# Kernel tuning notes

Hardware: AMD Instinct MI355X
Metric: run time of the kernel (lower is better)

Reference implementation:

```python
import jax, jax.numpy as jnp
import numpy as np

B = 1024
P = 8
D = 2048
NUM_IDS = 64
MARGIN = 0.3
EPS = 1e-12


def setup_inputs() -> dict:
    key = jax.random.key(0)
    k1, k2, k3 = jax.random.split(key, 3)
    feats = jax.random.normal(k1, (B, P * D), dtype=jnp.float32)
    labels = jax.random.randint(k2, (B,), 0, NUM_IDS, dtype=jnp.int64)
    subs = jax.random.randint(k3, (B,), 0, 2, dtype=jnp.int64)
    return {"feats": feats, "labels": labels, "subs": subs}


def reference(feats, labels, subs):
    b = feats.shape[0]
    f = feats.reshape(b, -1, D)  # [B, P, D]
    dt = f.dtype

    # Per-sample class centers via a single segment-mean pass
    # (equivalent to the original per-sample boolean-mask mean loop).
    seg_sum = jax.ops.segment_sum(f, labels, num_segments=NUM_IDS)  # [NUM_IDS, P, D]
    counts = jax.ops.segment_sum(jnp.ones((b,), dt), labels, num_segments=NUM_IDS)
    centers_by_id = seg_sum / jnp.maximum(counts, 1.0)[:, None, None]
    centers = centers_by_id[labels]  # [B, P, D]

    # dist_ap[i] = sum_p ||f[i,p] - center[i,p]||
    d_ap = jnp.sqrt(jnp.clip(jnp.sum((f - centers) ** 2, axis=-1), EPS, None)).sum(-1)  # [B]
    dist_ap = d_ap[:, None] + d_ap[None, :]  # [B, B]

    # pairwise_distance: dist_aa[i,j] = sum_p ||f[i,p] - f[j,p]||, via gemm trick
    sq = jnp.sum(f * f, axis=-1)  # [B, P]
    inner = jnp.einsum('ipd,jpd->ijp', f, f)  # [B, B, P]
    d2 = sq[:, None, :] + sq[None, :, :] - 2.0 * inner
    dist_aa = jnp.sqrt(jnp.clip(d2, EPS, None)).sum(-1)  # [B, B]

    # masked margin loss over negative (different-label) pairs
    mask = labels[:, None] != labels[None, :]  # [B, B] bool
    vals = jnp.clip(dist_ap - dist_aa + MARGIN, 0.0, None)
    maskf = mask.astype(dt)
    loss = jnp.sum(vals * maskf) / jnp.sum(maskf)
    return loss
```

## Files before the change

kernel.cpp:

```cpp
#include <hip/hip_runtime.h>
#include <hip/hip_bf16.h>

#define B_ 1024
#define P_ 8
#define D_ 2048
#define FD_ (P_ * D_)
#define NID 64
#define MARGIN_ 0.3f
#define EPS_ 1e-12f

typedef unsigned short u16;
typedef float float4_t __attribute__((ext_vector_type(4)));

#define AS1 __attribute__((address_space(1)))
#define AS3 __attribute__((address_space(3)))

__device__ __forceinline__ float bf2f(u16 v) {
    unsigned x = (unsigned)v << 16;
    float f;
    __builtin_memcpy(&f, &x, 4);
    return f;
}

static const size_t OFF_COUNTS = 0;
static const size_t OFF_OFFS   = 256;
static const size_t OFF_PERM   = 512;
static const size_t OFF_NEG    = 4608;
static const size_t OFF_DONE   = 4616;
static const size_t OFF_POS    = 8176;
static const size_t OFF_S      = 8192;
static const size_t OFF_SQ     = 40960;
static const size_t OFF_DAP    = 73728;
static const size_t OFF_FB     = 131072;
static const size_t OFF_PD     = OFF_FB + (size_t)B_ * FD_;

__global__ void k_prep(const float* __restrict__ feats, const int* __restrict__ labels,
                       unsigned char* __restrict__ fb, float* __restrict__ sq,
                       float* countsf, int* offs, int* perm, float* negcnt,
                       float* S, float* possum, int* done) {
    int tid = threadIdx.x;
    if (blockIdx.x < B_) {
        int i = blockIdx.x;
        int w = tid >> 6, lane = tid & 63;
        const float* frow = feats + (size_t)i * FD_;
        unsigned char* brow = fb + (size_t)i * FD_;
#pragma unroll
        for (int pp = 0; pp < 2; pp++) {
            int p = w * 2 + pp;
            int off = p * D_;
            float s2 = 0.f;
#pragma unroll
            for (int ch = 0; ch < 8; ch++) {
                int d = off + ch * 256 + lane * 4;
                float4 f = *(const float4*)(frow + d);
                int pk = __builtin_amdgcn_cvt_pk_fp8_f32(f.x, f.y, 0, false);
                pk = __builtin_amdgcn_cvt_pk_fp8_f32(f.z, f.w, pk, true);
                *(unsigned int*)(brow + d) = (unsigned int)pk;
                s2 += f.x * f.x + f.y * f.y + f.z * f.z + f.w * f.w;
            }
            for (int o = 32; o; o >>= 1) s2 += __shfl_down(s2, o, 64);
            if (lane == 0) sq[i * P_ + p] = s2;
        }
        return;
    }
    __shared__ int h[NID], o[NID], cur[NID];
    if (tid < NID) h[tid] = 0;
    __syncthreads();
    for (int i = tid; i < B_; i += 256) atomicAdd(&h[labels[i]], 1);
    __syncthreads();
    if (tid == 0) {
        int acc = 0;
        long long ss = 0;
        for (int c = 0; c < NID; c++) {
            o[c] = acc;
            acc += h[c];
            ss += (long long)h[c] * h[c];
        }
        *negcnt = (float)((long long)B_ * B_ - ss);
        *possum = 0.f;
        done[0] = 0;
    }
    __syncthreads();
    if (tid < NID) {
        countsf[tid] = (float)h[tid];
        offs[tid] = o[tid];
        cur[tid] = o[tid];
    }
    __syncthreads();
    for (int i = tid; i < B_; i += 256) {
        int pos = atomicAdd(&cur[labels[i]], 1);
        perm[pos] = i;
    }
    for (int i = tid; i < B_ * P_; i += 256) S[i] = 0.f;
}

__global__ __launch_bounds__(512, 4) void k_pairs(const unsigned char* __restrict__ fb,
                                                  const float* __restrict__ sq,
                                                  const int* __restrict__ labels,
                                                  float* __restrict__ S,
                                                  u16* __restrict__ pd) {
    const int i0 = blockIdx.y * 128, j0 = blockIdx.x * 128;
    const int p = blockIdx.z;
    __shared__ __align__(16) unsigned char smem[65536];
    __shared__ float sqAs[128], sqBs[128];
    __shared__ int labA[128], labB[128];
    const int tid = threadIdx.x;
    const int lane = tid & 63, wid = tid >> 6;
    const int s = wid & 3, h = wid >> 2;
    if (tid < 128) {
        sqAs[tid] = sq[(i0 + tid) * 8 + p];
        labA[tid] = labels[i0 + tid];
    } else if (tid < 256) {
        int t = tid - 128;
        sqBs[t] = sq[(j0 + t) * 8 + p];
        labB[t] = labels[j0 + t];
    }

    const int wi = (s >> 1) * 64, wj = (s & 1) * 64;
    const int lhi = lane >> 4, llo = lane & 15;
    const int sl = llo & 7;
    const int lr = lane >> 3;
    const int lc = (lane & 7) ^ lr;

    unsigned char* const As = smem + h * 16384;
    unsigned char* const Bs = smem + 32768 + h * 16384;

    const size_t colbase = (size_t)p * D_ + (size_t)h * 1024 + (size_t)lc * 16;
    const unsigned char* gA[4];
    const unsigned char* gB[4];
    unsigned char* lA[4];
    unsigned char* lB[4];
#pragma unroll
    for (int inst = 0; inst < 4; inst++) {
        int r0 = s * 32 + inst * 8;
        gA[inst] = fb + (size_t)(i0 + r0 + lr) * FD_ + colbase;
        gB[inst] = fb + (size_t)(j0 + r0 + lr) * FD_ + colbase;
        lA[inst] = As + r0 * 128;
        lB[inst] = Bs + r0 * 128;
    }

    float4_t acc[4][4];
#pragma unroll
    for (int a = 0; a < 4; a++)
#pragma unroll
        for (int b = 0; b < 4; b++) acc[a][b] = (float4_t){0.f, 0.f, 0.f, 0.f};

    for (int kb = 0; kb < 8; kb++) {
        const int koff = kb * 128;
        __syncthreads();
#pragma unroll
        for (int inst = 0; inst < 4; inst++) {
            __builtin_amdgcn_global_load_lds((const AS1 void*)(gA[inst] + koff),
                                             (AS3 void*)lA[inst], 16, 0, 0);
            __builtin_amdgcn_global_load_lds((const AS1 void*)(gB[inst] + koff),
                                             (AS3 void*)lB[inst], 16, 0, 0);
        }
        __syncthreads();
#pragma unroll
        for (int ks = 0; ks < 4; ks++) {
            const int pcb = ((2 * ks + (lhi >> 1)) ^ sl) * 16 + (lhi & 1) * 8;
            long af[4], bf[4];
#pragma unroll
            for (int a = 0; a < 4; a++) {
                af[a] = *(const long*)(As + (wi + a * 16 + llo) * 128 + pcb);
                bf[a] = *(const long*)(Bs + (wj + a * 16 + llo) * 128 + pcb);
            }
#pragma unroll
            for (int a = 0; a < 4; a++)
#pragma unroll
                for (int b = 0; b < 4; b++)
                    acc[a][b] = __builtin_amdgcn_mfma_f32_16x16x32_fp8_fp8(
                        af[a], bf[b], acc[a][b], 0, 0, 0);
        }
    }
    __syncthreads();
    float* ep = (float*)smem;
    if (h == 1) {
#pragma unroll
        for (int a = 0; a < 4; a++)
#pragma unroll
            for (int b = 0; b < 4; b++)
                *(float4_t*)&ep[(((s * 4 + a) * 4 + b) * 64 + lane) * 4] = acc[a][b];
    }
    __syncthreads();
    if (h == 0) {
        u16* outp = pd + (size_t)p * B_ * B_;
        float rs[4][4];
#pragma unroll
        for (int a = 0; a < 4; a++)
#pragma unroll
            for (int r = 0; r < 4; r++) rs[a][r] = 0.f;
#pragma unroll
        for (int a = 0; a < 4; a++) {
            int la0 = labA[wi + a * 16 + lhi * 4 + 0];
            int la1 = labA[wi + a * 16 + lhi * 4 + 1];
            int la2 = labA[wi + a * 16 + lhi * 4 + 2];
            int la3 = labA[wi + a * 16 + lhi * 4 + 3];
#pragma unroll
            for (int b = 0; b < 4; b++) {
                float4_t o = *(const float4_t*)&ep[(((s * 4 + a) * 4 + b) * 64 + lane) * 4];
                int lb = labB[wj + b * 16 + llo];
                int jl = wj + b * 16 + llo;
#pragma unroll
                for (int r = 0; r < 4; r++) {
                    int il = wi + a * 16 + lhi * 4 + r;
                    float t = acc[a][b][r] + o[r];
                    float d2 = sqAs[il] + sqBs[jl] - 2.0f * t;
                    outp[(size_t)(i0 + il) * B_ + (j0 + jl)] =
                        __bfloat16_as_ushort(__float2bfloat16(sqrtf(fmaxf(d2, EPS_))));
                    int la = (r == 0) ? la0 : (r == 1) ? la1 : (r == 2) ? la2 : la3;
                    if (lb == la) rs[a][r] += t;
                }
            }
        }
#pragma unroll
        for (int a = 0; a < 4; a++)
#pragma unroll
            for (int r = 0; r < 4; r++) {
                float v = rs[a][r];
                v += __shfl_xor(v, 1, 64);
                v += __shfl_xor(v, 2, 64);
                v += __shfl_xor(v, 4, 64);
                v += __shfl_xor(v, 8, 64);
                if (llo == 0)
                    atomicAdd(&S[(size_t)(i0 + wi + a * 16 + lhi * 4 + r) * 8 + p], v);
            }
    }
}

__global__ void k_dap(const float* __restrict__ S, const float* __restrict__ sq,
                      const float* __restrict__ countsf, const int* __restrict__ offs,
                      const int* __restrict__ perm, float* __restrict__ dap) {
    int c = blockIdx.x;
    int tid = threadIdx.x;
    int cnt = (int)countsf[c];
    int off = offs[c];
    __shared__ float T[8];
    if (tid < 8) {
        float t = 0.f;
        for (int m = 0; m < cnt; m++) t += S[(size_t)perm[off + m] * 8 + tid];
        T[tid] = t;
    }
    __syncthreads();
    float n = fmaxf((float)cnt, 1.f);
    float inv = 1.f / n, inv2 = inv * inv;
    for (int m = tid; m < cnt; m += 64) {
        int i = perm[off + m];
        float d = 0.f;
#pragma unroll
        for (int p = 0; p < 8; p++) {
            float d2 = sq[i * 8 + p] - 2.f * inv * S[(size_t)i * 8 + p] + inv2 * T[p];
            d += sqrtf(fmaxf(d2, EPS_));
        }
        dap[i] = d;
    }
}

__global__ void k_lossred(const u16* __restrict__ pd, const float* __restrict__ dap,
                          const int* __restrict__ labels, float* possum,
                          const float* __restrict__ negcnt, int* __restrict__ done,
                          float* __restrict__ out) {
    int i = blockIdx.x;
    int tid = threadIdx.x;
    float di = dap[i];
    int li = labels[i];
    int j0 = tid * 4;
    float d0 = 0.f, d1 = 0.f, d2 = 0.f, d3 = 0.f;
#pragma unroll
    for (int p = 0; p < P_; p++) {
        ushort4 v = *(const ushort4*)&pd[(size_t)p * B_ * B_ + (size_t)i * B_ + j0];
        d0 += bf2f(v.x);
        d1 += bf2f(v.y);
        d2 += bf2f(v.z);
        d3 += bf2f(v.w);
    }
    int4 lj = *(const int4*)&labels[j0];
    float4 dj = *(const float4*)&dap[j0];
    float lsum = 0.f;
    if (lj.x != li) lsum += fmaxf(di + dj.x - d0 + MARGIN_, 0.f);
    if (lj.y != li) lsum += fmaxf(di + dj.y - d1 + MARGIN_, 0.f);
    if (lj.z != li) lsum += fmaxf(di + dj.z - d2 + MARGIN_, 0.f);
    if (lj.w != li) lsum += fmaxf(di + dj.w - d3 + MARGIN_, 0.f);
    for (int o = 32; o; o >>= 1) lsum += __shfl_down(lsum, o, 64);
    __shared__ float red[4];
    int wid = tid >> 6, lane = tid & 63;
    if (lane == 0) red[wid] = lsum;
    __syncthreads();
    if (tid == 0) {
        atomicAdd(possum, red[0] + red[1] + red[2] + red[3]);
        __threadfence();
        int v = atomicAdd(done, 1);
        if (v == B_ - 1) {
            float ps = atomicAdd(possum, 0.f);
            out[0] = ps / negcnt[0];
        }
    }
}

extern "C" void kernel_launch(void* const* d_in, const int* in_sizes, int n_in,
                              void* d_out, int out_size, void* d_ws, size_t ws_size,
                              hipStream_t stream) {
    const float* feats = (const float*)d_in[0];
    const int* labels  = (const int*)d_in[1];
    float* out = (float*)d_out;

    char* w = (char*)d_ws;
    float* countsf = (float*)(w + OFF_COUNTS);
    int* offs      = (int*)(w + OFF_OFFS);
    int* perm      = (int*)(w + OFF_PERM);
    float* negcnt  = (float*)(w + OFF_NEG);
    int* done      = (int*)(w + OFF_DONE);
    float* possum  = (float*)(w + OFF_POS);
    float* S       = (float*)(w + OFF_S);
    float* sq      = (float*)(w + OFF_SQ);
    float* dap     = (float*)(w + OFF_DAP);
    unsigned char* fb = (unsigned char*)(w + OFF_FB);
    u16* pd        = (u16*)(w + OFF_PD);

    k_prep<<<B_ + 1, 256, 0, stream>>>(feats, labels, fb, sq, countsf, offs, perm,
                                       negcnt, S, possum, done);
    k_pairs<<<dim3(8, 8, 8), 512, 0, stream>>>(fb, sq, labels, S, pd);
    k_dap<<<NID, 64, 0, stream>>>(S, sq, countsf, offs, perm, dap);
    k_lossred<<<B_, 256, 0, stream>>>(pd, dap, labels, possum, negcnt, done, out);
}
```

Baseline: 166.8 us.

## Exploit Gram symmetry: compute upper-triangle tiles and mirror outputs

The pairwise FP8 GEMM now covers only upper-triangular 128x64 tile pairs per part (576 jobs instead of 512 full 128x128 tiles). Each off-diagonal tile writes its distances twice, once transposed, and also accumulates same-label column sums into S for the mirrored rows. The block shrinks to 256 threads and the shared-memory footprint is reduced. This roughly halves the MFMA and feature-load work. In exchange, the transposed bf16 stores are strided and poorly coalesced, there are extra atomics, and the block shape is smaller.

```diff
diff --git a/kernel.cpp b/kernel.cpp
--- a/kernel.cpp
+++ b/kernel.cpp
@@ -8,6 +8,7 @@
 #define NID 64
 #define MARGIN_ 0.3f
 #define EPS_ 1e-12f
+#define NJOBS 576
 
 typedef unsigned short u16;
 typedef float float4_t __attribute__((ext_vector_type(4)));
@@ -94,48 +95,58 @@
     for (int i = tid; i < B_ * P_; i += 256) S[i] = 0.f;
 }
 
-__global__ __launch_bounds__(512, 4) void k_pairs(const unsigned char* __restrict__ fb,
+__global__ __launch_bounds__(256, 3) void k_pairs(const unsigned char* __restrict__ fb,
                                                   const float* __restrict__ sq,
                                                   const int* __restrict__ labels,
                                                   float* __restrict__ S,
                                                   u16* __restrict__ pd) {
-    const int i0 = blockIdx.y * 128, j0 = blockIdx.x * 128;
-    const int p = blockIdx.z;
-    __shared__ __align__(16) unsigned char smem[65536];
-    __shared__ float sqAs[128], sqBs[128];
-    __shared__ int labA[128], labB[128];
+    int t = blockIdx.x >> 3;
+    const int p = blockIdx.x & 7;
+    int ti = 0;
+    while (t >= 16 - 2 * ti) { t -= 16 - 2 * ti; ti++; }
+    const int ju = 2 * ti + t;
+    const int i0 = ti * 128, j0 = ju * 64;
+    const bool offdiag = (ju >= 2 * ti + 2);
+
+    __shared__ __align__(16) unsigned char smem[49152];
+    __shared__ float sqAs[128], sqBs[64];
+    __shared__ int labA[128], labB[64];
     const int tid = threadIdx.x;
     const int lane = tid & 63, wid = tid >> 6;
-    const int s = wid & 3, h = wid >> 2;
+    const int s = wid & 1, h = wid >> 1;
     if (tid < 128) {
         sqAs[tid] = sq[(i0 + tid) * 8 + p];
         labA[tid] = labels[i0 + tid];
-    } else if (tid < 256) {
-        int t = tid - 128;
-        sqBs[t] = sq[(j0 + t) * 8 + p];
-        labB[t] = labels[j0 + t];
-    }
-
-    const int wi = (s >> 1) * 64, wj = (s & 1) * 64;
+    } else if (tid < 192) {
+        int u = tid - 128;
+        sqBs[u] = sq[(j0 + u) * 8 + p];
+        labB[u] = labels[j0 + u];
+    }
+
+    const int wi = s * 64;
     const int lhi = lane >> 4, llo = lane & 15;
     const int sl = llo & 7;
     const int lr = lane >> 3;
     const int lc = (lane & 7) ^ lr;
 
     unsigned char* const As = smem + h * 16384;
-    unsigned char* const Bs = smem + 32768 + h * 16384;
+    unsigned char* const Bs = smem + 32768 + h * 8192;
 
     const size_t colbase = (size_t)p * D_ + (size_t)h * 1024 + (size_t)lc * 16;
-    const unsigned char* gA[4];
+    const unsigned char* gA[8];
+    unsigned char* lA[8];
     const unsigned char* gB[4];
-    unsigned char* lA[4];
     unsigned char* lB[4];
+#pragma unroll
+    for (int inst = 0; inst < 8; inst++) {
+        int r0 = s * 64 + inst * 8;
+        gA[inst] = fb + (size_t)(i0 + r0 + lr) * FD_ + colbase;
+        lA[inst] = As + r0 * 128;
+    }
 #pragma unroll
     for (int inst = 0; inst < 4; inst++) {
         int r0 = s * 32 + inst * 8;
-        gA[inst] = fb + (size_t)(i0 + r0 + lr) * FD_ + colbase;
         gB[inst] = fb + (size_t)(j0 + r0 + lr) * FD_ + colbase;
-        lA[inst] = As + r0 * 128;
         lB[inst] = Bs + r0 * 128;
     }
 
@@ -149,12 +160,13 @@
         const int koff = kb * 128;
         __syncthreads();
 #pragma unroll
-        for (int inst = 0; inst < 4; inst++) {
+        for (int inst = 0; inst < 8; inst++)
             __builtin_amdgcn_global_load_lds((const AS1 void*)(gA[inst] + koff),
                                              (AS3 void*)lA[inst], 16, 0, 0);
+#pragma unroll
+        for (int inst = 0; inst < 4; inst++)
             __builtin_amdgcn_global_load_lds((const AS1 void*)(gB[inst] + koff),
                                              (AS3 void*)lB[inst], 16, 0, 0);
-        }
         __syncthreads();
 #pragma unroll
         for (int ks = 0; ks < 4; ks++) {
@@ -163,7 +175,7 @@
 #pragma unroll
             for (int a = 0; a < 4; a++) {
                 af[a] = *(const long*)(As + (wi + a * 16 + llo) * 128 + pcb);
-                bf[a] = *(const long*)(Bs + (wj + a * 16 + llo) * 128 + pcb);
+                bf[a] = *(const long*)(Bs + (a * 16 + llo) * 128 + pcb);
             }
 #pragma unroll
             for (int a = 0; a < 4; a++)
@@ -186,10 +198,13 @@
     if (h == 0) {
         u16* outp = pd + (size_t)p * B_ * B_;
         float rs[4][4];
+        float cs[4];
 #pragma unroll
         for (int a = 0; a < 4; a++)
 #pragma unroll
             for (int r = 0; r < 4; r++) rs[a][r] = 0.f;
+#pragma unroll
+        for (int b = 0; b < 4; b++) cs[b] = 0.f;
 #pragma unroll
         for (int a = 0; a < 4; a++) {
             int la0 = labA[wi + a * 16 + lhi * 4 + 0];
@@ -199,17 +214,21 @@
 #pragma unroll
             for (int b = 0; b < 4; b++) {
                 float4_t o = *(const float4_t*)&ep[(((s * 4 + a) * 4 + b) * 64 + lane) * 4];
-                int lb = labB[wj + b * 16 + llo];
-                int jl = wj + b * 16 + llo;
+                int jl = b * 16 + llo;
+                int lb = labB[jl];
 #pragma unroll
                 for (int r = 0; r < 4; r++) {
                     int il = wi + a * 16 + lhi * 4 + r;
-                    float t = acc[a][b][r] + o[r];
-                    float d2 = sqAs[il] + sqBs[jl] - 2.0f * t;
-                    outp[(size_t)(i0 + il) * B_ + (j0 + jl)] =
-                        __bfloat16_as_ushort(__float2bfloat16(sqrtf(fmaxf(d2, EPS_))));
+                    float tt = acc[a][b][r] + o[r];
+                    float d2 = sqAs[il] + sqBs[jl] - 2.0f * tt;
+                    u16 bv = __bfloat16_as_ushort(__float2bfloat16(sqrtf(fmaxf(d2, EPS_))));
+                    outp[(size_t)(i0 + il) * B_ + (j0 + jl)] = bv;
+                    if (offdiag) outp[(size_t)(j0 + jl) * B_ + (i0 + il)] = bv;
                     int la = (r == 0) ? la0 : (r == 1) ? la1 : (r == 2) ? la2 : la3;
-                    if (lb == la) rs[a][r] += t;
+                    if (lb == la) {
+                        rs[a][r] += tt;
+                        if (offdiag) cs[b] += tt;
+                    }
                 }
             }
         }
@@ -225,6 +244,16 @@
                 if (llo == 0)
                     atomicAdd(&S[(size_t)(i0 + wi + a * 16 + lhi * 4 + r) * 8 + p], v);
             }
+        if (offdiag) {
+#pragma unroll
+            for (int b = 0; b < 4; b++) {
+                float v = cs[b];
+                v += __shfl_xor(v, 16, 64);
+                v += __shfl_xor(v, 32, 64);
+                if (lhi == 0)
+                    atomicAdd(&S[(size_t)(j0 + b * 16 + llo) * 8 + p], v);
+            }
+        }
     }
 }
 
@@ -319,7 +348,7 @@
 
     k_prep<<<B_ + 1, 256, 0, stream>>>(feats, labels, fb, sq, countsf, offs, perm,
                                        negcnt, S, possum, done);
-    k_pairs<<<dim3(8, 8, 8), 512, 0, stream>>>(fb, sq, labels, S, pd);
+    k_pairs<<<NJOBS, 256, 0, stream>>>(fb, sq, labels, S, pd);
     k_dap<<<NID, 64, 0, stream>>>(S, sq, countsf, offs, perm, dap);
     k_lossred<<<B_, 256, 0, stream>>>(pd, dap, labels, possum, negcnt, done, out);
 }
```

New measurement: 167.8 us. About the same (+0.6%).

## Drop intra-block split-K in pair GEMM, use 4 waves over full K

Applied to the files above, without the earlier changes.

The pair-distance kernel previously used 8 waves split into two halves that each handled half of the K dimension, then combined partial accumulators through shared memory before the epilogue. Now 4 waves each process the full K range over 16 iterations, which removes the LDS reduction, two barriers, and the idle epilogue half, and halves shared memory use. In exchange there are fewer waves per block to hide load latency and twice as many serialized K steps per block.

```diff
diff --git a/kernel.cpp b/kernel.cpp
--- a/kernel.cpp
+++ b/kernel.cpp
@@ -94,45 +94,44 @@
     for (int i = tid; i < B_ * P_; i += 256) S[i] = 0.f;
 }
 
-__global__ __launch_bounds__(512, 4) void k_pairs(const unsigned char* __restrict__ fb,
+__global__ __launch_bounds__(256, 4) void k_pairs(const unsigned char* __restrict__ fb,
                                                   const float* __restrict__ sq,
                                                   const int* __restrict__ labels,
                                                   float* __restrict__ S,
                                                   u16* __restrict__ pd) {
     const int i0 = blockIdx.y * 128, j0 = blockIdx.x * 128;
     const int p = blockIdx.z;
-    __shared__ __align__(16) unsigned char smem[65536];
+    __shared__ __align__(16) unsigned char smem[32768];
     __shared__ float sqAs[128], sqBs[128];
     __shared__ int labA[128], labB[128];
     const int tid = threadIdx.x;
-    const int lane = tid & 63, wid = tid >> 6;
-    const int s = wid & 3, h = wid >> 2;
+    const int lane = tid & 63, w = tid >> 6;
+    const int wr = w >> 1, wc = w & 1;
     if (tid < 128) {
         sqAs[tid] = sq[(i0 + tid) * 8 + p];
         labA[tid] = labels[i0 + tid];
-    } else if (tid < 256) {
+    } else {
         int t = tid - 128;
         sqBs[t] = sq[(j0 + t) * 8 + p];
         labB[t] = labels[j0 + t];
     }
 
-    const int wi = (s >> 1) * 64, wj = (s & 1) * 64;
     const int lhi = lane >> 4, llo = lane & 15;
     const int sl = llo & 7;
     const int lr = lane >> 3;
     const int lc = (lane & 7) ^ lr;
 
-    unsigned char* const As = smem + h * 16384;
-    unsigned char* const Bs = smem + 32768 + h * 16384;
-
-    const size_t colbase = (size_t)p * D_ + (size_t)h * 1024 + (size_t)lc * 16;
+    unsigned char* const As = smem;
+    unsigned char* const Bs = smem + 16384;
+
+    const size_t colbase = (size_t)p * D_ + (size_t)lc * 16;
     const unsigned char* gA[4];
     const unsigned char* gB[4];
     unsigned char* lA[4];
     unsigned char* lB[4];
 #pragma unroll
     for (int inst = 0; inst < 4; inst++) {
-        int r0 = s * 32 + inst * 8;
+        int r0 = w * 32 + inst * 8;
         gA[inst] = fb + (size_t)(i0 + r0 + lr) * FD_ + colbase;
         gB[inst] = fb + (size_t)(j0 + r0 + lr) * FD_ + colbase;
         lA[inst] = As + r0 * 128;
@@ -145,7 +144,7 @@
 #pragma unroll
         for (int b = 0; b < 4; b++) acc[a][b] = (float4_t){0.f, 0.f, 0.f, 0.f};
 
-    for (int kb = 0; kb < 8; kb++) {
+    for (int kb = 0; kb < 16; kb++) {
         const int koff = kb * 128;
         __syncthreads();
 #pragma unroll
@@ -162,8 +161,8 @@
             long af[4], bf[4];
 #pragma unroll
             for (int a = 0; a < 4; a++) {
-                af[a] = *(const long*)(As + (wi + a * 16 + llo) * 128 + pcb);
-                bf[a] = *(const long*)(Bs + (wj + a * 16 + llo) * 128 + pcb);
+                af[a] = *(const long*)(As + (wr * 64 + a * 16 + llo) * 128 + pcb);
+                bf[a] = *(const long*)(Bs + (wc * 64 + a * 16 + llo) * 128 + pcb);
             }
 #pragma unroll
             for (int a = 0; a < 4; a++)
@@ -173,59 +172,47 @@
                         af[a], bf[b], acc[a][b], 0, 0, 0);
         }
     }
-    __syncthreads();
-    float* ep = (float*)smem;
-    if (h == 1) {
-#pragma unroll
-        for (int a = 0; a < 4; a++)
-#pragma unroll
-            for (int b = 0; b < 4; b++)
-                *(float4_t*)&ep[(((s * 4 + a) * 4 + b) * 64 + lane) * 4] = acc[a][b];
-    }
-    __syncthreads();
-    if (h == 0) {
-        u16* outp = pd + (size_t)p * B_ * B_;
-        float rs[4][4];
-#pragma unroll
-        for (int a = 0; a < 4; a++)
-#pragma unroll
-            for (int r = 0; r < 4; r++) rs[a][r] = 0.f;
-#pragma unroll
-        for (int a = 0; a < 4; a++) {
-            int la0 = labA[wi + a * 16 + lhi * 4 + 0];
-            int la1 = labA[wi + a * 16 + lhi * 4 + 1];
-            int la2 = labA[wi + a * 16 + lhi * 4 + 2];
-            int la3 = labA[wi + a * 16 + lhi * 4 + 3];
-#pragma unroll
-            for (int b = 0; b < 4; b++) {
-                float4_t o = *(const float4_t*)&ep[(((s * 4 + a) * 4 + b) * 64 + lane) * 4];
-                int lb = labB[wj + b * 16 + llo];
-                int jl = wj + b * 16 + llo;
-#pragma unroll
-                for (int r = 0; r < 4; r++) {
-                    int il = wi + a * 16 + lhi * 4 + r;
-                    float t = acc[a][b][r] + o[r];
-                    float d2 = sqAs[il] + sqBs[jl] - 2.0f * t;
-                    outp[(size_t)(i0 + il) * B_ + (j0 + jl)] =
-                        __bfloat16_as_ushort(__float2bfloat16(sqrtf(fmaxf(d2, EPS_))));
-                    int la = (r == 0) ? la0 : (r == 1) ? la1 : (r == 2) ? la2 : la3;
-                    if (lb == la) rs[a][r] += t;
-                }
+
+    u16* outp = pd + (size_t)p * B_ * B_;
+    float rs[4][4];
+#pragma unroll
+    for (int a = 0; a < 4; a++)
+#pragma unroll
+        for (int r = 0; r < 4; r++) rs[a][r] = 0.f;
+#pragma unroll
+    for (int a = 0; a < 4; a++) {
+        int la0 = labA[wr * 64 + a * 16 + lhi * 4 + 0];
+        int la1 = labA[wr * 64 + a * 16 + lhi * 4 + 1];
+        int la2 = labA[wr * 64 + a * 16 + lhi * 4 + 2];
+        int la3 = labA[wr * 64 + a * 16 + lhi * 4 + 3];
+#pragma unroll
+        for (int b = 0; b < 4; b++) {
+            int jl = wc * 64 + b * 16 + llo;
+            int lb = labB[jl];
+#pragma unroll
+            for (int r = 0; r < 4; r++) {
+                int il = wr * 64 + a * 16 + lhi * 4 + r;
+                float tt = acc[a][b][r];
+                float d2 = sqAs[il] + sqBs[jl] - 2.0f * tt;
+                outp[(size_t)(i0 + il) * B_ + (j0 + jl)] =
+                    __bfloat16_as_ushort(__float2bfloat16(sqrtf(fmaxf(d2, EPS_))));
+                int la = (r == 0) ? la0 : (r == 1) ? la1 : (r == 2) ? la2 : la3;
+                if (lb == la) rs[a][r] += tt;
             }
         }
-#pragma unroll
-        for (int a = 0; a < 4; a++)
-#pragma unroll
-            for (int r = 0; r < 4; r++) {
-                float v = rs[a][r];
-                v += __shfl_xor(v, 1, 64);
-                v += __shfl_xor(v, 2, 64);
-                v += __shfl_xor(v, 4, 64);
-                v += __shfl_xor(v, 8, 64);
-                if (llo == 0)
-                    atomicAdd(&S[(size_t)(i0 + wi + a * 16 + lhi * 4 + r) * 8 + p], v);
-            }
-    }
+    }
+#pragma unroll
+    for (int a = 0; a < 4; a++)
+#pragma unroll
+        for (int r = 0; r < 4; r++) {
+            float v = rs[a][r];
+            v += __shfl_xor(v, 1, 64);
+            v += __shfl_xor(v, 2, 64);
+            v += __shfl_xor(v, 4, 64);
+            v += __shfl_xor(v, 8, 64);
+            if (llo == 0)
+                atomicAdd(&S[(size_t)(i0 + wr * 64 + a * 16 + lhi * 4 + r) * 8 + p], v);
+        }
 }
 
 __global__ void k_dap(const float* __restrict__ S, const float* __restrict__ sq,
@@ -319,7 +306,7 @@
 
     k_prep<<<B_ + 1, 256, 0, stream>>>(feats, labels, fb, sq, countsf, offs, perm,
                                        negcnt, S, possum, done);
-    k_pairs<<<dim3(8, 8, 8), 512, 0, stream>>>(fb, sq, labels, S, pd);
+    k_pairs<<<dim3(8, 8, 8), 256, 0, stream>>>(fb, sq, labels, S, pd);
     k_dap<<<NID, 64, 0, stream>>>(S, sq, countsf, offs, perm, dap);
     k_lossred<<<B_, 256, 0, stream>>>(pd, dap, labels, possum, negcnt, done, out);
 }
```

Measured after the change: 167.8 us. Within noise of the previous version (+0.6%).
